# Kernel optimization log

Measured on AMD Instinct MI355X. Metric: run time of the kernel, lower is better.

Reference implementation:

```python
import jax, jax.numpy as jnp
import numpy as np

NEG_SLOPE = 0.01  # torch leaky_relu default

def leaky_relu(x):
    return jnp.where(x >= 0, x, NEG_SLOPE * x)

def setup_inputs() -> dict:
    key = jax.random.key(0)
    ks = jax.random.split(key, 12)
    N, E = 100000, 800000
    C_in, C_edge, pre, H, hs, C_out = 64, 32, 96, 4, 24, 128
    aggr_out = H * hs + 1  # count=True appends in-degree column
    x = jax.random.normal(ks[0], (N, C_in), dtype=jnp.float32)
    edge_attr = jax.random.normal(ks[1], (E, C_edge), dtype=jnp.float32)
    edge_index = jax.random.randint(ks[2], (2, E), 0, N, dtype=jnp.int32)
    s = 0.05
    W_pre = jax.random.normal(ks[3], (C_in + C_edge, pre), dtype=jnp.float32) * s
    b_pre = jax.random.normal(ks[4], (pre,), dtype=jnp.float32) * s
    W_att = jax.random.normal(ks[5], (pre, H), dtype=jnp.float32) * s
    b_att = jax.random.normal(ks[6], (H,), dtype=jnp.float32) * s
    W_val = jax.random.normal(ks[7], (pre, H * hs), dtype=jnp.float32) * s
    b_val = jax.random.normal(ks[8], (H * hs,), dtype=jnp.float32) * s
    W_out = jax.random.normal(ks[9], (C_in + aggr_out, C_out), dtype=jnp.float32) * s
    b_out = jax.random.normal(ks[10], (C_out,), dtype=jnp.float32) * s
    return {"x": x, "edge_attr": edge_attr, "edge_index": edge_index,
            "W_pre": W_pre, "b_pre": b_pre, "W_att": W_att, "b_att": b_att,
            "W_val": W_val, "b_val": b_val, "W_out": W_out, "b_out": b_out}

def reference(x, edge_attr, edge_index, W_pre, b_pre, W_att, b_att, W_val, b_val, W_out, b_out):
    N = x.shape[0]
    src, dst = edge_index[0], edge_index[1]
    H = W_att.shape[1]
    hs = W_val.shape[1] // H
    # gather + pre MLP: [E, in+edge] -> [E, pre]
    msg = jnp.concatenate([x[src], edge_attr], axis=-1)
    msg = leaky_relu(msg @ W_pre + b_pre)
    # multi-head attention aggregation keyed by destination
    logits = msg @ W_att + b_att                       # [E, H]
    vals = (msg @ W_val + b_val).reshape(-1, H, hs)    # [E, H, hs]
    seg_max = jax.ops.segment_max(logits, dst, num_segments=N)      # [N, H]
    seg_max = jnp.where(jnp.isfinite(seg_max), seg_max, 0.0)
    alpha = jnp.exp(logits - seg_max[dst])                          # [E, H]
    denom = jax.ops.segment_sum(alpha, dst, num_segments=N)         # [N, H]
    alpha = alpha / denom[dst]
    agg = jax.ops.segment_sum(alpha[:, :, None] * vals, dst, num_segments=N)  # [N, H, hs]
    agg = agg.reshape(N, H * hs)
    count = jax.ops.segment_sum(jnp.ones((src.shape[0], 1), dtype=x.dtype), dst, num_segments=N)
    messages = jnp.concatenate([agg, count], axis=-1)
    out = jnp.concatenate([x, messages], axis=-1)
    return leaky_relu(out @ W_out + b_out)
```

## Files before the change

kernel.cpp:

```cpp
#include <hip/hip_runtime.h>


#define NEG 0.01f

__device__ __forceinline__ float lrelu(float v) { return v > 0.f ? v : NEG * v; }

__device__ __forceinline__ unsigned bfpack2(float a, float b) {
    unsigned ua = __float_as_uint(a); ua = (ua + 0x7fff + ((ua >> 16) & 1)) >> 16;
    unsigned ub = __float_as_uint(b); ub = (ub + 0x7fff + ((ub >> 16) & 1)) >> 16;
    return ua | (ub << 16);
}

__global__ void zero_kernel(float* __restrict__ p, long n) {
    long i = ((long)blockIdx.x * 256 + threadIdx.x) * 4;
    if (i + 3 < n) {
        *(float4*)(p + i) = make_float4(0.f, 0.f, 0.f, 0.f);
    } else {
        for (long k = i; k < n; ++k) p[k] = 0.f;
    }
}

__global__ void hist_kernel(const int* __restrict__ ei, int* __restrict__ cnt, int E) {
    int e = blockIdx.x * 256 + threadIdx.x;
    if (e < E) atomicAdd(&cnt[ei[E + e]], 1);
}

__global__ __launch_bounds__(1024)
void scan_kernel(const int* __restrict__ cnt, int* __restrict__ offs,
                 int* __restrict__ curs, int N) {
    __shared__ int ls[1024];
    int tid = threadIdx.x;
    int chunk = (N + 1023) >> 10;
    int lo = tid * chunk;
    int hi = lo + chunk; if (hi > N) hi = N; if (lo > N) lo = N;
    int s = 0;
    for (int i = lo; i < hi; ++i) s += cnt[i];
    ls[tid] = s;
    __syncthreads();
    for (int off = 1; off < 1024; off <<= 1) {
        int v = 0;
        if (tid >= off) v = ls[tid - off];
        __syncthreads();
        ls[tid] += v;
        __syncthreads();
    }
    int run = ls[tid] - s;
    for (int i = lo; i < hi; ++i) {
        offs[i] = run; curs[i] = run; run += cnt[i];
    }
}

__global__ __launch_bounds__(256)
void blocksum_kernel(const int* __restrict__ cnt, int* __restrict__ bsum, int N) {
    int base = blockIdx.x * 1024;
    int tid = threadIdx.x;
    int v = 0;
#pragma unroll
    for (int r = 0; r < 4; ++r) {
        int idx = base + r * 256 + tid;
        if (idx < N) v += cnt[idx];
    }
#pragma unroll
    for (int d = 32; d > 0; d >>= 1) v += __shfl_down(v, d, 64);
    __shared__ int ws[4];
    int wv = tid >> 6, lane = tid & 63;
    if (lane == 0) ws[wv] = v;
    __syncthreads();
    if (tid == 0) bsum[blockIdx.x] = ws[0] + ws[1] + ws[2] + ws[3];
}

__global__ __launch_bounds__(1024)
void bscan_kernel(int* __restrict__ bsum, int NB) {
    __shared__ int ls[1024];
    int tid = threadIdx.x;
    int v = (tid < NB) ? bsum[tid] : 0;
    ls[tid] = v;
    __syncthreads();
    for (int off = 1; off < 1024; off <<= 1) {
        int t = 0;
        if (tid >= off) t = ls[tid - off];
        __syncthreads();
        ls[tid] += t;
        __syncthreads();
    }
    if (tid < NB) bsum[tid] = ls[tid] - v;
}

__global__ __launch_bounds__(1024)
void offs_kernel(const int* __restrict__ cnt, const int* __restrict__ boff,
                 int* __restrict__ offs, int* __restrict__ curs, int N) {
    int tid = threadIdx.x;
    int i = blockIdx.x * 1024 + tid;
    int lane = tid & 63, wv = tid >> 6;
    int c = (i < N) ? cnt[i] : 0;
    int v = c;
#pragma unroll
    for (int d = 1; d < 64; d <<= 1) {
        int t = __shfl_up(v, d, 64);
        if (lane >= d) v += t;
    }
    __shared__ int ws[16];
    if (lane == 63) ws[wv] = v;
    __syncthreads();
    if (wv == 0) {
        int wvv = (lane < 16) ? ws[lane] : 0;
#pragma unroll
        for (int d = 1; d < 16; d <<= 1) {
            int t = __shfl_up(wvv, d, 64);
            if (lane >= d) wvv += t;
        }
        if (lane < 16) ws[lane] = wvv;
    }
    __syncthreads();
    int waveoff = (wv > 0) ? ws[wv - 1] : 0;
    int excl = v - c + waveoff + boff[blockIdx.x];
    if (i < N) { offs[i] = excl; curs[i] = excl; }
}

__global__ __launch_bounds__(256, 4)
void pre_kernel(const float* __restrict__ x, const float* __restrict__ Wp,
                const float* __restrict__ bp, float* __restrict__ U, int N)
{
    __shared__ float xs[64][65];
    int n0 = blockIdx.x * 64;
    for (int p = threadIdx.x; p < 64 * 16; p += 256) {
        int row = p >> 4, f4 = p & 15;
        int n = n0 + row;
        float4 v = make_float4(0.f, 0.f, 0.f, 0.f);
        if (n < N) v = ((const float4*)(x + (long)n * 64))[f4];
        xs[row][f4 * 4 + 0] = v.x; xs[row][f4 * 4 + 1] = v.y;
        xs[row][f4 * 4 + 2] = v.z; xs[row][f4 * 4 + 3] = v.w;
    }
    __syncthreads();

    int node = threadIdx.x >> 2;
    int cg = threadIdx.x & 3;
    float4 acc[6];
#pragma unroll
    for (int c = 0; c < 6; ++c) acc[c] = ((const float4*)(bp + cg * 24))[c];
    for (int k = 0; k < 64; ++k) {
        float xv = xs[node][k];
        const float* wr = Wp + k * 96 + cg * 24;
#pragma unroll
        for (int c = 0; c < 6; ++c) {
            float4 w = ((const float4*)wr)[c];
            acc[c].x += xv * w.x; acc[c].y += xv * w.y;
            acc[c].z += xv * w.z; acc[c].w += xv * w.w;
        }
    }
    int n = n0 + node;
    if (n < N) {
#pragma unroll
        for (int c = 0; c < 6; ++c)
            ((float4*)(U + (long)n * 96 + cg * 24))[c] = acc[c];
    }
}

__global__ __launch_bounds__(256, 1)
void edge_msg_kernel(const float* __restrict__ U, const float* __restrict__ ea,
                     const int* __restrict__ ei,
                     const float* __restrict__ Wp,
                     const float* __restrict__ Wa, const float* __restrict__ ba,
                     unsigned* __restrict__ vals, int* __restrict__ curs,
                     int* __restrict__ eidx, int E)
{
    __shared__ __attribute__((aligned(16))) unsigned pool[2 * 64 * 52];
    float* easf = (float*)pool;
    float* exf  = (float*)pool + 4608;

    int lane = threadIdx.x & 63;
    int wid  = threadIdx.x >> 6;
    int half = __builtin_amdgcn_readfirstlane(wid & 1);
    int pl   = __builtin_amdgcn_readfirstlane(wid >> 1);
    int pt   = (wid & 1) * 64 + lane;
    long pairBase = ((long)blockIdx.x * 2 + pl) * 64;
    int e = (int)(pairBase + lane);
    bool active = (e < E);
    int ec = active ? e : (E - 1);
    int src = ei[ec];
    int dst = ei[E + ec];

    {
        const float4* gea = (const float4*)ea;
        long g0 = pairBase * 8;
        long gmax = (long)E * 8;
#pragma unroll
        for (int i = 0; i < 4; ++i) {
            int idx = i * 128 + pt;
            long gi = g0 + idx;
            float4 v = make_float4(0.f, 0.f, 0.f, 0.f);
            if (gi < gmax) v = gea[gi];
            int ed = idx >> 3, f4 = idx & 7;
            *(float4*)(easf + ((pl * 64 + ed) * 36 + f4 * 4)) = v;
        }
    }

    if (half == 0 && active) {
        int pos = atomicAdd(&curs[dst], 1);
        eidx[pos] = e;
    }
    __syncthreads();

    float4 S[12];
    const float4* Urow = (const float4*)(U + (long)src * 96 + half * 48);
#pragma unroll
    for (int j = 0; j < 12; ++j) S[j] = Urow[j];

    const float* Wh = Wp + 64 * 96 + half * 48;

#pragma unroll 1
    for (int kc = 0; kc < 8; ++kc) {
        float4 c = *(const float4*)(easf + ((pl * 64 + lane) * 36 + kc * 4));
        const float* W0 = Wh + (4 * kc + 0) * 96;
        const float* W1 = Wh + (4 * kc + 1) * 96;
        const float* W2 = Wh + (4 * kc + 2) * 96;
        const float* W3 = Wh + (4 * kc + 3) * 96;
#pragma unroll
        for (int j = 0; j < 12; ++j) {
            float4 w0 = ((const float4*)W0)[j];
            float4 w1 = ((const float4*)W1)[j];
            float4 w2 = ((const float4*)W2)[j];
            float4 w3 = ((const float4*)W3)[j];
            S[j].x += c.x * w0.x + c.y * w1.x + c.z * w2.x + c.w * w3.x;
            S[j].y += c.x * w0.y + c.y * w1.y + c.z * w2.y + c.w * w3.y;
            S[j].z += c.x * w0.z + c.y * w1.z + c.z * w2.z + c.w * w3.z;
            S[j].w += c.x * w0.w + c.y * w1.w + c.z * w2.w + c.w * w3.w;
        }
    }
#pragma unroll
    for (int j = 0; j < 12; ++j) {
        S[j].x = lrelu(S[j].x); S[j].y = lrelu(S[j].y);
        S[j].z = lrelu(S[j].z); S[j].w = lrelu(S[j].w);
    }

    float l0 = 0.f, l1 = 0.f, l2 = 0.f, l3 = 0.f;
    const float* Wah = Wa + half * 48 * 4;
#pragma unroll
    for (int j = 0; j < 12; ++j) {
        float4 m = S[j];
        float4 w0 = ((const float4*)(Wah + (4 * j + 0) * 4))[0];
        float4 w1 = ((const float4*)(Wah + (4 * j + 1) * 4))[0];
        float4 w2 = ((const float4*)(Wah + (4 * j + 2) * 4))[0];
        float4 w3 = ((const float4*)(Wah + (4 * j + 3) * 4))[0];
        l0 += m.x * w0.x + m.y * w1.x + m.z * w2.x + m.w * w3.x;
        l1 += m.x * w0.y + m.y * w1.y + m.z * w2.y + m.w * w3.y;
        l2 += m.x * w0.z + m.y * w1.z + m.z * w2.z + m.w * w3.z;
        l3 += m.x * w0.w + m.y * w1.w + m.z * w2.w + m.w * w3.w;
    }

    if (half == 0) {
        exf[0 * 128 + pl * 64 + lane] = l0;
        exf[1 * 128 + pl * 64 + lane] = l1;
        exf[2 * 128 + pl * 64 + lane] = l2;
        exf[3 * 128 + pl * 64 + lane] = l3;
    }
    __syncthreads();
    if (half == 1) {
        l0 += exf[0 * 128 + pl * 64 + lane];
        l1 += exf[1 * 128 + pl * 64 + lane];
        l2 += exf[2 * 128 + pl * 64 + lane];
        l3 += exf[3 * 128 + pl * 64 + lane];
    }
    __syncthreads();

    if (active) {
        unsigned* srow = pool + ((pl * 64 + lane) * 52) + half * 24;
#pragma unroll
        for (int j2 = 0; j2 < 6; ++j2) {
            uint4 u;
            u.x = bfpack2(S[2 * j2].x,     S[2 * j2].y);
            u.y = bfpack2(S[2 * j2].z,     S[2 * j2].w);
            u.z = bfpack2(S[2 * j2 + 1].x, S[2 * j2 + 1].y);
            u.w = bfpack2(S[2 * j2 + 1].z, S[2 * j2 + 1].w);
            *(uint4*)(srow + j2 * 4) = u;
        }
        if (half == 1) {
            float p0 = __expf(l0 + ba[0]), p1 = __expf(l1 + ba[1]);
            float p2 = __expf(l2 + ba[2]), p3 = __expf(l3 + ba[3]);
            *(uint4*)(pool + ((pl * 64 + lane) * 52) + 48) =
                make_uint4(__float_as_uint(p0), __float_as_uint(p1),
                           __float_as_uint(p2), __float_as_uint(p3));
        }
    }
    __syncthreads();

    {
        long nval = (long)E - pairBase;
        if (nval > 64) nval = 64;
        if (nval > 0) {
            int tot = (int)nval * 13;
            uint4* dst4 = (uint4*)(vals + pairBase * 52);
            const uint4* src4 = (const uint4*)(pool + pl * 64 * 52);
            for (int i = pt; i < tot; i += 128)
                dst4[i] = src4[i];
        }
    }
}

__global__ __launch_bounds__(512)
void gather_kernel(const unsigned* __restrict__ vals, const int* __restrict__ offs,
                   const int* __restrict__ cnt, const int* __restrict__ eidx,
                   const float* __restrict__ Wv, const float* __restrict__ bv,
                   float* __restrict__ agg, float* __restrict__ cntF, int N)
{
    __shared__ __attribute__((aligned(16))) float Wvs[96][96];
    __shared__ float Tls[8][4][96];
    int wv = threadIdx.x >> 6;
    int lane = threadIdx.x & 63;

    for (int i = threadIdx.x; i < 96 * 24; i += 512)
        ((float4*)Wvs)[i] = ((const float4*)Wv)[i];
    __syncthreads();

    int nbase = blockIdx.x * 64 + wv * 8;

#pragma unroll 1
    for (int it = 0; it < 8; ++it) {
        int node = nbase + it;
        bool nvalid = (node < N);
        int start = nvalid ? offs[node] : 0;
        int deg   = nvalid ? cnt[node] : 0;

        float s0[4] = {0.f, 0.f, 0.f, 0.f};
        float s1[4] = {0.f, 0.f, 0.f, 0.f};
        float d0 = 0.f, d1 = 0.f, d2 = 0.f, d3 = 0.f;
        if (lane < 52) {
#define PROC(v) {                                                   \
            float vf = __uint_as_float(v);                          \
            float q0 = __shfl(vf, 48, 64);                          \
            float q1 = __shfl(vf, 49, 64);                          \
            float q2 = __shfl(vf, 50, 64);                          \
            float q3 = __shfl(vf, 51, 64);                          \
            float m0 = __uint_as_float((v) << 16);                  \
            float m1 = __uint_as_float((v) & 0xffff0000u);          \
            s0[0] += q0 * m0; s1[0] += q0 * m1;                     \
            s0[1] += q1 * m0; s1[1] += q1 * m1;                     \
            s0[2] += q2 * m0; s1[2] += q2 * m1;                     \
            s0[3] += q3 * m0; s1[3] += q3 * m1;                     \
            d0 += q0; d1 += q1; d2 += q2; d3 += q3; }
            const int* eix = eidx + start;
            int r = 0;
            for (; r + 4 <= deg; r += 4) {
                long o0 = (long)eix[r]     * 52;
                long o1 = (long)eix[r + 1] * 52;
                long o2 = (long)eix[r + 2] * 52;
                long o3 = (long)eix[r + 3] * 52;
                unsigned va = vals[o0 + lane];
                unsigned vb = vals[o1 + lane];
                unsigned vc = vals[o2 + lane];
                unsigned vd = vals[o3 + lane];
                PROC(va) PROC(vb) PROC(vc) PROC(vd)
            }
            for (; r < deg; ++r) {
                unsigned v = vals[(long)eix[r] * 52 + lane];
                PROC(v)
            }
#undef PROC
        }
        if (lane < 48) {
            float r0 = (deg > 0) ? 1.f / d0 : 0.f;
            float r1 = (deg > 0) ? 1.f / d1 : 0.f;
            float r2 = (deg > 0) ? 1.f / d2 : 0.f;
            float r3 = (deg > 0) ? 1.f / d3 : 0.f;
            Tls[wv][0][2 * lane] = s0[0] * r0; Tls[wv][0][2 * lane + 1] = s1[0] * r0;
            Tls[wv][1][2 * lane] = s0[1] * r1; Tls[wv][1][2 * lane + 1] = s1[1] * r1;
            Tls[wv][2][2 * lane] = s0[2] * r2; Tls[wv][2][2 * lane + 1] = s1[2] * r2;
            Tls[wv][3][2 * lane] = s0[3] * r3; Tls[wv][3][2 * lane + 1] = s1[3] * r3;
        }
        if (nvalid) {
            if (lane < 48) {
                int j = 2 * lane;
                int h = lane / 12;
                float a0 = bv[j], a1 = bv[j + 1];
                const float* Th = &Tls[wv][h][0];
#pragma unroll 4
                for (int k = 0; k < 96; ++k) {
                    float t = Th[k];
                    float2 w = *(const float2*)&Wvs[k][j];
                    a0 += t * w.x; a1 += t * w.y;
                }
                float2 o = (deg > 0) ? make_float2(a0, a1) : make_float2(0.f, 0.f);
                *(float2*)(agg + (long)node * 96 + j) = o;
            } else if (lane == 48) {
                cntF[node] = (float)deg;
            }
        }
    }
}

__global__ __launch_bounds__(256, 4)
void node_kernel(const float* __restrict__ x, const float* __restrict__ aggW,
                 const float* __restrict__ cntF,
                 const float* __restrict__ Wo, const float* __restrict__ bo,
                 float* __restrict__ out, int N)
{
    __shared__ float s_in[161][68];
    int n0 = blockIdx.x * 64;
    int j0 = blockIdx.y * 64;

    for (int idx = threadIdx.x; idx < 64 * 16; idx += 256) {
        int row = idx >> 4, f4 = idx & 15;
        int n = n0 + row;
        float4 v = make_float4(0.f, 0.f, 0.f, 0.f);
        if (n < N) v = ((const float4*)(x + (long)n * 64))[f4];
        s_in[4 * f4 + 0][row] = v.x; s_in[4 * f4 + 1][row] = v.y;
        s_in[4 * f4 + 2][row] = v.z; s_in[4 * f4 + 3][row] = v.w;
    }
    for (int idx = threadIdx.x; idx < 64 * 24; idx += 256) {
        int row = idx / 24, c4 = idx % 24;
        int n = n0 + row;
        float4 v = make_float4(0.f, 0.f, 0.f, 0.f);
        if (n < N) v = ((const float4*)(aggW + (long)n * 96))[c4];
        s_in[64 + 4 * c4 + 0][row] = v.x; s_in[64 + 4 * c4 + 1][row] = v.y;
        s_in[64 + 4 * c4 + 2][row] = v.z; s_in[64 + 4 * c4 + 3][row] = v.w;
    }
    if (threadIdx.x < 64) {
        int n = n0 + threadIdx.x;
        s_in[160][threadIdx.x] = (n < N) ? cntF[n] : 0.f;
    }
    __syncthreads();

    int tj = threadIdx.x & 15;
    int tn = threadIdx.x >> 4;
    float acc[4][4];
#pragma unroll
    for (int i = 0; i < 4; ++i)
#pragma unroll
        for (int c = 0; c < 4; ++c) acc[i][c] = 0.f;

    const float* Wcol = Wo + j0 + tj * 4;
    for (int k = 0; k < 161; ++k) {
        float4 w  = *(const float4*)(Wcol + (long)k * 128);
        float4 iv = *(const float4*)&s_in[k][tn * 4];
        acc[0][0] += iv.x * w.x; acc[0][1] += iv.x * w.y; acc[0][2] += iv.x * w.z; acc[0][3] += iv.x * w.w;
        acc[1][0] += iv.y * w.x; acc[1][1] += iv.y * w.y; acc[1][2] += iv.y * w.z; acc[1][3] += iv.y * w.w;
        acc[2][0] += iv.z * w.x; acc[2][1] += iv.z * w.y; acc[2][2] += iv.z * w.z; acc[2][3] += iv.z * w.w;
        acc[3][0] += iv.w * w.x; acc[3][1] += iv.w * w.y; acc[3][2] += iv.w * w.z; acc[3][3] += iv.w * w.w;
    }
    float4 b = *(const float4*)(bo + j0 + tj * 4);
#pragma unroll
    for (int i = 0; i < 4; ++i) {
        int n = n0 + tn * 4 + i;
        if (n < N) {
            float4 o;
            o.x = lrelu(acc[i][0] + b.x);
            o.y = lrelu(acc[i][1] + b.y);
            o.z = lrelu(acc[i][2] + b.z);
            o.w = lrelu(acc[i][3] + b.w);
            *(float4*)(out + (long)n * 128 + j0 + tj * 4) = o;
        }
    }
}

__global__ __launch_bounds__(256, 1)
void edge_atm_kernel(const float* __restrict__ x, const float* __restrict__ ea,
                     const int* __restrict__ ei,
                     const float* __restrict__ Wp, const float* __restrict__ bp,
                     const float* __restrict__ Wa, const float* __restrict__ ba,
                     const float* __restrict__ Wv, const float* __restrict__ bv,
                     float* __restrict__ aggW, float* __restrict__ denomW,
                     float* __restrict__ cntW, int E)
{
    int e = blockIdx.x * 256 + threadIdx.x;
    if (e >= E) return;
    int src = ei[e];
    int dst = ei[E + e];
    float4 S[24];
#pragma unroll
    for (int j = 0; j < 24; ++j) S[j] = ((const float4*)bp)[j];
    const float* xrow = x + (long)src * 64;
    const float* erow = ea + (long)e * 32;
#pragma unroll 1
    for (int kc = 0; kc < 6; ++kc) {
        const float* sp = (kc < 4) ? (xrow + kc * 16) : (erow + (kc - 4) * 16);
        const float* Wb = Wp + kc * 16 * 96;
#pragma unroll 1
        for (int i = 0; i < 4; ++i) {
            float4 cc = ((const float4*)sp)[i];
#pragma unroll
            for (int j = 0; j < 24; ++j) {
                float4 w0 = ((const float4*)(Wb + (4 * i + 0) * 96))[j];
                float4 w1 = ((const float4*)(Wb + (4 * i + 1) * 96))[j];
                float4 w2 = ((const float4*)(Wb + (4 * i + 2) * 96))[j];
                float4 w3 = ((const float4*)(Wb + (4 * i + 3) * 96))[j];
                S[j].x += cc.x * w0.x + cc.y * w1.x + cc.z * w2.x + cc.w * w3.x;
                S[j].y += cc.x * w0.y + cc.y * w1.y + cc.z * w2.y + cc.w * w3.y;
                S[j].z += cc.x * w0.z + cc.y * w1.z + cc.z * w2.z + cc.w * w3.z;
                S[j].w += cc.x * w0.w + cc.y * w1.w + cc.z * w2.w + cc.w * w3.w;
            }
        }
    }
#pragma unroll
    for (int j = 0; j < 24; ++j) {
        S[j].x = lrelu(S[j].x); S[j].y = lrelu(S[j].y);
        S[j].z = lrelu(S[j].z); S[j].w = lrelu(S[j].w);
    }
    float l0 = ba[0], l1 = ba[1], l2 = ba[2], l3 = ba[3];
#pragma unroll
    for (int j = 0; j < 24; ++j) {
        float4 m = S[j];
        float4 w0 = ((const float4*)(Wa + (4 * j + 0) * 4))[0];
        float4 w1 = ((const float4*)(Wa + (4 * j + 1) * 4))[0];
        float4 w2 = ((const float4*)(Wa + (4 * j + 2) * 4))[0];
        float4 w3 = ((const float4*)(Wa + (4 * j + 3) * 4))[0];
        l0 += m.x * w0.x + m.y * w1.x + m.z * w2.x + m.w * w3.x;
        l1 += m.x * w0.y + m.y * w1.y + m.z * w2.y + m.w * w3.y;
        l2 += m.x * w0.z + m.y * w1.z + m.z * w2.z + m.w * w3.z;
        l3 += m.x * w0.w + m.y * w1.w + m.z * w2.w + m.w * w3.w;
    }
    float p0 = __expf(l0), p1 = __expf(l1), p2 = __expf(l2), p3 = __expf(l3);
    float* aggp = aggW + (long)dst * 96;
#pragma unroll 1
    for (int j4 = 0; j4 < 24; ++j4) {
        float4 acc = ((const float4*)bv)[j4];
        const float* Wc = Wv + 4 * j4;
#pragma unroll
        for (int j = 0; j < 24; ++j) {
            float4 m = S[j];
            float4 w0 = ((const float4*)(Wc + (4 * j + 0) * 96))[0];
            float4 w1 = ((const float4*)(Wc + (4 * j + 1) * 96))[0];
            float4 w2 = ((const float4*)(Wc + (4 * j + 2) * 96))[0];
            float4 w3 = ((const float4*)(Wc + (4 * j + 3) * 96))[0];
            acc.x += m.x * w0.x + m.y * w1.x + m.z * w2.x + m.w * w3.x;
            acc.y += m.x * w0.y + m.y * w1.y + m.z * w2.y + m.w * w3.y;
            acc.z += m.x * w0.z + m.y * w1.z + m.z * w2.z + m.w * w3.z;
            acc.w += m.x * w0.w + m.y * w1.w + m.z * w2.w + m.w * w3.w;
        }
        float ph = (j4 < 6) ? p0 : (j4 < 12) ? p1 : (j4 < 18) ? p2 : p3;
        unsafeAtomicAdd(aggp + 4 * j4 + 0, ph * acc.x);
        unsafeAtomicAdd(aggp + 4 * j4 + 1, ph * acc.y);
        unsafeAtomicAdd(aggp + 4 * j4 + 2, ph * acc.z);
        unsafeAtomicAdd(aggp + 4 * j4 + 3, ph * acc.w);
    }
    float* dn = denomW + (long)dst * 4;
    unsafeAtomicAdd(dn + 0, p0);
    unsafeAtomicAdd(dn + 1, p1);
    unsafeAtomicAdd(dn + 2, p2);
    unsafeAtomicAdd(dn + 3, p3);
    unsafeAtomicAdd(cntW + dst, 1.0f);
}

__global__ __launch_bounds__(256, 4)
void node_atm_kernel(const float* __restrict__ x, const float* __restrict__ aggW,
                     const float* __restrict__ denomW, const float* __restrict__ cntW,
                     const float* __restrict__ Wo, const float* __restrict__ bo,
                     float* __restrict__ out, int N)
{
    __shared__ float s_in[161][64];
    int n0 = blockIdx.x * 64;
    int j0 = blockIdx.y * 64;
    for (int p = threadIdx.x; p < 161 * 64; p += 256) {
        int k = p >> 6, nl = p & 63;
        int n = n0 + nl;
        float v = 0.f;
        if (n < N) {
            if (k < 64) v = x[(long)n * 64 + k];
            else if (k < 160) {
                int kk = k - 64;
                float d = denomW[n * 4 + (kk / 24)];
                v = d > 0.f ? aggW[(long)n * 96 + kk] / d : 0.f;
            } else v = cntW[n];
        }
        s_in[k][nl] = v;
    }
    __syncthreads();
    int tj = threadIdx.x & 15;
    int tn = threadIdx.x >> 4;
    float acc[4][4];
#pragma unroll
    for (int i = 0; i < 4; ++i)
#pragma unroll
        for (int c = 0; c < 4; ++c) acc[i][c] = 0.f;
    const float* Wcol = Wo + j0 + tj * 4;
    for (int k = 0; k < 161; ++k) {
        float4 w  = *(const float4*)(Wcol + (long)k * 128);
        float4 iv = *(const float4*)&s_in[k][tn * 4];
        acc[0][0] += iv.x * w.x; acc[0][1] += iv.x * w.y; acc[0][2] += iv.x * w.z; acc[0][3] += iv.x * w.w;
        acc[1][0] += iv.y * w.x; acc[1][1] += iv.y * w.y; acc[1][2] += iv.y * w.z; acc[1][3] += iv.y * w.w;
        acc[2][0] += iv.z * w.x; acc[2][1] += iv.z * w.y; acc[2][2] += iv.z * w.z; acc[2][3] += iv.z * w.w;
        acc[3][0] += iv.w * w.x; acc[3][1] += iv.w * w.y; acc[3][2] += iv.w * w.z; acc[3][3] += iv.w * w.w;
    }
    float4 b = *(const float4*)(bo + j0 + tj * 4);
#pragma unroll
    for (int i = 0; i < 4; ++i) {
        int n = n0 + tn * 4 + i;
        if (n < N) {
            float4 o;
            o.x = lrelu(acc[i][0] + b.x);
            o.y = lrelu(acc[i][1] + b.y);
            o.z = lrelu(acc[i][2] + b.z);
            o.w = lrelu(acc[i][3] + b.w);
            *(float4*)(out + (long)n * 128 + j0 + tj * 4) = o;
        }
    }
}

extern "C" void kernel_launch(void* const* d_in, const int* in_sizes, int n_in,
                              void* d_out, int out_size, void* d_ws, size_t ws_size,
                              hipStream_t stream)
{
    const float* x  = (const float*)d_in[0];
    const float* ea = (const float*)d_in[1];
    const int*   ei = (const int*)d_in[2];
    const float* Wp = (const float*)d_in[3];
    const float* bp = (const float*)d_in[4];
    const float* Wa = (const float*)d_in[5];
    const float* ba = (const float*)d_in[6];
    const float* Wv = (const float*)d_in[7];
    const float* bv = (const float*)d_in[8];
    const float* Wo = (const float*)d_in[9];
    const float* bo = (const float*)d_in[10];
    float* out = (float*)d_out;

    int N = in_sizes[0] / 64;
    int E = in_sizes[2] / 2;
    int NB = (N + 1023) / 1024;

    size_t need = (size_t)E * 52 * 4 + (size_t)N * 96 * 4 + (size_t)N * 4 * 4
                + (size_t)NB * 4 + (size_t)E * 4;

    if (ws_size >= need) {
        unsigned* vals = (unsigned*)d_ws;
        float* Uagg = (float*)(vals + (long)E * 52);
        float* cntF = Uagg + (long)N * 96;
        int*   cnti = (int*)(cntF + N);
        int*   offs = cnti + N;
        int*   curs = offs + N;
        int*   bsum = curs + N;
        int*   eidx = bsum + NB;

        hipMemsetAsync(cnti, 0, (size_t)N * sizeof(int), stream);
        hist_kernel<<<(E + 255) / 256, 256, 0, stream>>>(ei, cnti, E);
        if (NB <= 1024) {
            blocksum_kernel<<<NB, 256, 0, stream>>>(cnti, bsum, N);
            bscan_kernel<<<1, 1024, 0, stream>>>(bsum, NB);
            offs_kernel<<<NB, 1024, 0, stream>>>(cnti, bsum, offs, curs, N);
        } else {
            scan_kernel<<<1, 1024, 0, stream>>>(cnti, offs, curs, N);
        }
        pre_kernel<<<(N + 63) / 64, 256, 0, stream>>>(x, Wp, bp, Uagg, N);
        edge_msg_kernel<<<(2 * E + 255) / 256, 256, 0, stream>>>(
            Uagg, ea, ei, Wp, Wa, ba, vals, curs, eidx, E);
        gather_kernel<<<(N + 63) / 64, 512, 0, stream>>>(
            vals, offs, cnti, eidx, Wv, bv, Uagg, cntF, N);
        dim3 ng((N + 63) / 64, 2);
        node_kernel<<<ng, 256, 0, stream>>>(x, Uagg, cntF, Wo, bo, out, N);
    } else {
        float* aggW   = (float*)d_ws;
        float* denomW = aggW + (long)N * 96;
        float* cntW   = denomW + (long)N * 4;
        long zn = (long)N * 101;
        int  zb = (int)(((zn + 3) / 4 + 255) / 256);
        zero_kernel<<<zb, 256, 0, stream>>>(aggW, zn);
        edge_atm_kernel<<<(E + 255) / 256, 256, 0, stream>>>(
            x, ea, ei, Wp, bp, Wa, ba, Wv, bv, aggW, denomW, cntW, E);
        dim3 ng((N + 63) / 64, 2);
        node_atm_kernel<<<ng, 256, 0, stream>>>(x, aggW, denomW, cntW, Wo, bo, out, N);
    }
}
```

Measured before the change: 723.7 us.

## Process two nodes per wave in gather kernel and batch value projection

```diff
diff --git a/kernel.cpp b/kernel.cpp
--- a/kernel.cpp
+++ b/kernel.cpp
@@ -304,7 +304,7 @@
                    float* __restrict__ agg, float* __restrict__ cntF, int N)
 {
     __shared__ __attribute__((aligned(16))) float Wvs[96][96];
-    __shared__ float Tls[8][4][96];
+    __shared__ float Tls[8][2][4][96];
     int wv = threadIdx.x >> 6;
     int lane = threadIdx.x & 63;
 
@@ -312,14 +312,16 @@
         ((float4*)Wvs)[i] = ((const float4*)Wv)[i];
     __syncthreads();
 
-    int nbase = blockIdx.x * 64 + wv * 8;
+    int nodeA = blockIdx.x * 16 + wv * 2;
+    int degAB[2];
 
 #pragma unroll 1
-    for (int it = 0; it < 8; ++it) {
-        int node = nbase + it;
+    for (int sub = 0; sub < 2; ++sub) {
+        int node = nodeA + sub;
         bool nvalid = (node < N);
         int start = nvalid ? offs[node] : 0;
         int deg   = nvalid ? cnt[node] : 0;
+        degAB[sub] = deg;
 
         float s0[4] = {0.f, 0.f, 0.f, 0.f};
         float s1[4] = {0.f, 0.f, 0.f, 0.f};
@@ -362,29 +364,40 @@
             float r1 = (deg > 0) ? 1.f / d1 : 0.f;
             float r2 = (deg > 0) ? 1.f / d2 : 0.f;
             float r3 = (deg > 0) ? 1.f / d3 : 0.f;
-            Tls[wv][0][2 * lane] = s0[0] * r0; Tls[wv][0][2 * lane + 1] = s1[0] * r0;
-            Tls[wv][1][2 * lane] = s0[1] * r1; Tls[wv][1][2 * lane + 1] = s1[1] * r1;
-            Tls[wv][2][2 * lane] = s0[2] * r2; Tls[wv][2][2 * lane + 1] = s1[2] * r2;
-            Tls[wv][3][2 * lane] = s0[3] * r3; Tls[wv][3][2 * lane + 1] = s1[3] * r3;
-        }
-        if (nvalid) {
-            if (lane < 48) {
-                int j = 2 * lane;
-                int h = lane / 12;
-                float a0 = bv[j], a1 = bv[j + 1];
-                const float* Th = &Tls[wv][h][0];
+            Tls[wv][sub][0][2 * lane] = s0[0] * r0; Tls[wv][sub][0][2 * lane + 1] = s1[0] * r0;
+            Tls[wv][sub][1][2 * lane] = s0[1] * r1; Tls[wv][sub][1][2 * lane + 1] = s1[1] * r1;
+            Tls[wv][sub][2][2 * lane] = s0[2] * r2; Tls[wv][sub][2][2 * lane + 1] = s1[2] * r2;
+            Tls[wv][sub][3][2 * lane] = s0[3] * r3; Tls[wv][sub][3][2 * lane + 1] = s1[3] * r3;
+        }
+    }
+
+    int degA = degAB[0], degB = degAB[1];
+    if (lane < 48) {
+        int j = 2 * lane;
+        int h = lane / 12;
+        float a0A = bv[j], a1A = bv[j + 1];
+        float a0B = a0A,  a1B = a1A;
+        const float* ThA = &Tls[wv][0][h][0];
+        const float* ThB = &Tls[wv][1][h][0];
 #pragma unroll 4
-                for (int k = 0; k < 96; ++k) {
-                    float t = Th[k];
-                    float2 w = *(const float2*)&Wvs[k][j];
-                    a0 += t * w.x; a1 += t * w.y;
-                }
-                float2 o = (deg > 0) ? make_float2(a0, a1) : make_float2(0.f, 0.f);
-                *(float2*)(agg + (long)node * 96 + j) = o;
-            } else if (lane == 48) {
-                cntF[node] = (float)deg;
-            }
-        }
+        for (int k = 0; k < 96; ++k) {
+            float2 w = *(const float2*)&Wvs[k][j];
+            float tA = ThA[k];
+            float tB = ThB[k];
+            a0A += tA * w.x; a1A += tA * w.y;
+            a0B += tB * w.x; a1B += tB * w.y;
+        }
+        if (nodeA < N) {
+            float2 o = (degA > 0) ? make_float2(a0A, a1A) : make_float2(0.f, 0.f);
+            *(float2*)(agg + (long)nodeA * 96 + j) = o;
+        }
+        if (nodeA + 1 < N) {
+            float2 o = (degB > 0) ? make_float2(a0B, a1B) : make_float2(0.f, 0.f);
+            *(float2*)(agg + (long)(nodeA + 1) * 96 + j) = o;
+        }
+    } else if (lane == 48) {
+        if (nodeA < N)     cntF[nodeA]     = (float)degA;
+        if (nodeA + 1 < N) cntF[nodeA + 1] = (float)degB;
     }
 }
 
@@ -641,7 +654,7 @@
         pre_kernel<<<(N + 63) / 64, 256, 0, stream>>>(x, Wp, bp, Uagg, N);
         edge_msg_kernel<<<(2 * E + 255) / 256, 256, 0, stream>>>(
             Uagg, ea, ei, Wp, Wa, ba, vals, curs, eidx, E);
-        gather_kernel<<<(N + 63) / 64, 512, 0, stream>>>(
+        gather_kernel<<<(N + 15) / 16, 512, 0, stream>>>(
             vals, offs, cnti, eidx, Wv, bv, Uagg, cntF, N);
         dim3 ng((N + 63) / 64, 2);
         node_kernel<<<ng, 256, 0, stream>>>(x, Uagg, cntF, Wo, bo, out, N);
```

New measurement: 719.2 us. No clear change (-0.6%).
